# Kernel tuning notes

Hardware: AMD Instinct MI355X
Metric: run time of the kernel (lower is better)

Reference implementation:

```python
import jax, jax.numpy as jnp
import numpy as np

BETA = 0.25  # commitment loss weight (standard VQ-VAE)


def setup_inputs() -> dict:
    key = jax.random.key(0)
    ks = jax.random.split(key, 6)
    B, C, H, W = 8, 64, 64, 64
    K = 8192  # codebook size
    return {
        "z": jax.random.normal(ks[0], (B, C, H, W), dtype=jnp.float32),
        "pre_w": jax.random.normal(ks[1], (C, C), dtype=jnp.float32) * (1.0 / np.sqrt(C)),
        "pre_b": jax.random.normal(ks[2], (C,), dtype=jnp.float32) * 0.02,
        "emb": jax.random.normal(ks[3], (K, C), dtype=jnp.float32),
        "post_w": jax.random.normal(ks[4], (C, C), dtype=jnp.float32) * (1.0 / np.sqrt(C)),
        "post_b": jax.random.normal(ks[5], (C,), dtype=jnp.float32) * 0.02,
    }


def reference(z, pre_w, pre_b, emb, post_w, post_b):
    B, C, H, W = z.shape
    # pre_quant_conv: 1x1 conv == channel-mixing matmul
    ze = jnp.einsum("bchw,oc->bohw", z, pre_w) + pre_b[None, :, None, None]
    # flatten to tokens [N, C]
    zf = ze.transpose(0, 2, 3, 1).reshape(-1, C)
    # squared L2 distances to codebook: ||z||^2 - 2 z.e + ||e||^2
    d = (jnp.sum(zf * zf, axis=1, keepdims=True)
         - 2.0 * (zf @ emb.T)
         + jnp.sum(emb * emb, axis=1)[None, :])  # [N, K]
    idx = jnp.argmin(d, axis=1)  # [N]
    q = emb[idx].reshape(B, H, W, C).transpose(0, 3, 1, 2)  # [B,C,H,W]
    # VQ losses
    codebook_loss = jnp.mean((jax.lax.stop_gradient(ze) - q) ** 2)
    commit_loss = BETA * jnp.mean((ze - jax.lax.stop_gradient(q)) ** 2)
    loss = codebook_loss + commit_loss
    # straight-through estimator
    quant = ze + jax.lax.stop_gradient(q - ze)
    # post_quant_conv: 1x1 conv
    out = jnp.einsum("bchw,oc->bohw", quant, post_w) + post_b[None, :, None, None]
    return out, loss
```

## Files before the change

### kernel.cpp

```cpp
#include <hip/hip_runtime.h>
#include <stdint.h>

#define HW 4096
#define NTOK 32768
#define KCB 8192
#define YSPLIT 8
#define KCOV (KCB / YSPLIT)
#define NCHUNK (KCOV / 64)
#define MARGIN 0.01f

typedef __bf16 bf16x8 __attribute__((ext_vector_type(8)));
typedef float f32x16 __attribute__((ext_vector_type(16)));
typedef unsigned int uint;
typedef unsigned short u16;
typedef unsigned long long u64;

static __device__ inline u16 f2bf(float f) {
    uint u = __float_as_uint(f);
    return (u16)((u + 0x7FFFu + ((u >> 16) & 1u)) >> 16);
}
static __device__ inline float bf2f(u16 h) {
    return __uint_as_float(((uint)h) << 16);
}
static __device__ inline uint fsort(float f) {
    uint u = __float_as_uint(f);
    return u ^ ((uint)((int)u >> 31) | 0x80000000u);
}
static __device__ inline float funsort(uint s) {
    uint m = (s & 0x80000000u) ? 0x80000000u : 0xFFFFFFFFu;
    return __uint_as_float(s ^ m);
}

__global__ __launch_bounds__(256) void embprep_kernel(
    const float* __restrict__ emb, u16* __restrict__ embq,
    float* __restrict__ ee, int* __restrict__ flagcnt)
{
    const int t   = threadIdx.x;
    const int k   = blockIdx.x * 32 + (t >> 3);
    const int sub = t & 7;
    const float4* er = (const float4*)(emb + (size_t)k * 64 + sub * 8);
    float4 v0 = er[0], v1 = er[1];

    float s = v0.x*v0.x + v0.y*v0.y + v0.z*v0.z + v0.w*v0.w
            + v1.x*v1.x + v1.y*v1.y + v1.z*v1.z + v1.w*v1.w;
    s += __shfl_xor(s, 1, 64);
    s += __shfl_xor(s, 2, 64);
    s += __shfl_xor(s, 4, 64);
    if (sub == 0) ee[k] = s;

    float vals[8] = {-2.f*v0.x, -2.f*v0.y, -2.f*v0.z, -2.f*v0.w,
                     -2.f*v1.x, -2.f*v1.y, -2.f*v1.z, -2.f*v1.w};
    u16 hb[8], lb[8];
    #pragma unroll
    for (int c = 0; c < 8; ++c) {
        hb[c] = f2bf(vals[c]);
        lb[c] = f2bf(vals[c] - bf2f(hb[c]));
    }
    uint4 uh, ul;
    uh.x = (uint)hb[0] | ((uint)hb[1] << 16);
    uh.y = (uint)hb[2] | ((uint)hb[3] << 16);
    uh.z = (uint)hb[4] | ((uint)hb[5] << 16);
    uh.w = (uint)hb[6] | ((uint)hb[7] << 16);
    ul.x = (uint)lb[0] | ((uint)lb[1] << 16);
    ul.y = (uint)lb[2] | ((uint)lb[3] << 16);
    ul.z = (uint)lb[4] | ((uint)lb[5] << 16);
    ul.w = (uint)lb[6] | ((uint)lb[7] << 16);

    const int sw = k & 7;
    uint4* out = (uint4*)(embq + (size_t)k * 128);
    out[sub ^ sw]       = uh;
    out[(8 + sub) ^ sw] = ul;
    if (k == 0 && t == 0) *flagcnt = 0;
}

__global__ __launch_bounds__(256) void preconv_kernel(
    const float* __restrict__ z, const float* __restrict__ pre_w,
    const float* __restrict__ pre_b, u16* __restrict__ zq)
{
    __shared__ __attribute__((aligned(16))) float wt[64 * 64];
    __shared__ __attribute__((aligned(16))) float zt[64 * 64];
    __shared__ float bls[64];
    const int t = threadIdx.x;
    const int tok0 = blockIdx.x * 64;
    const int b    = tok0 >> 12;
    const int hw0  = tok0 & 4095;

    for (int i = t; i < 64 * 64; i += 256) {
        int o = i >> 6, c = i & 63;
        wt[c * 64 + o] = pre_w[i];
    }
    if (t < 64) bls[t] = pre_b[t];
    {
        const int tl = t & 63;
        #pragma unroll
        for (int rr = 0; rr < 16; ++rr) {
            const int c = (t >> 6) + rr * 4;
            zt[c * 64 + tl] = z[(size_t)b * (64 * HW) + (size_t)c * HW + hw0 + tl];
        }
    }
    __syncthreads();

    const int tok = t >> 2;
    const int og  = t & 3;
    const int n   = tok0 + tok;

    float acc[16];
    #pragma unroll
    for (int j = 0; j < 16; ++j) acc[j] = 0.f;

    for (int c = 0; c < 64; ++c) {
        const float zv = zt[c * 64 + tok];
        #pragma unroll
        for (int g = 0; g < 4; ++g) {
            float4 w4 = *(const float4*)(wt + c * 64 + og * 16 + g * 4);
            acc[g*4+0] = fmaf(zv, w4.x, acc[g*4+0]);
            acc[g*4+1] = fmaf(zv, w4.y, acc[g*4+1]);
            acc[g*4+2] = fmaf(zv, w4.z, acc[g*4+2]);
            acc[g*4+3] = fmaf(zv, w4.w, acc[g*4+3]);
        }
    }
    #pragma unroll
    for (int j = 0; j < 16; ++j) acc[j] += bls[og * 16 + j];

    uint uh[8], ul[8];
    #pragma unroll
    for (int j = 0; j < 8; ++j) {
        float v0 = acc[2*j], v1 = acc[2*j+1];
        u16 h0 = f2bf(v0), h1 = f2bf(v1);
        u16 l0 = f2bf(v0 - bf2f(h0)), l1 = f2bf(v1 - bf2f(h1));
        uh[j] = (uint)h0 | ((uint)h1 << 16);
        ul[j] = (uint)l0 | ((uint)l1 << 16);
    }
    uint4* zh = (uint4*)(zq + (size_t)n * 128 + og * 16);
    uint4* zl = (uint4*)(zq + (size_t)n * 128 + 64 + og * 16);
    zh[0] = *(uint4*)&uh[0]; zh[1] = *(uint4*)&uh[4];
    zl[0] = *(uint4*)&ul[0]; zl[1] = *(uint4*)&ul[4];
}

__global__ __launch_bounds__(256, 3) void dist_kernel(
    const u16* __restrict__ zq, const u16* __restrict__ embq,
    const float* __restrict__ ee, u64* __restrict__ halfkey,
    float* __restrict__ halfsec)
{
    __shared__ __attribute__((aligned(16))) char smem[32768];
    __shared__ u64 gbk[128];

    const int t    = threadIdx.x;
    const int w    = t >> 6;
    const int l    = t & 63;
    const int col  = l & 31;
    const int half = l >> 5;
    const int tok0 = blockIdx.x * 128;
    const int y    = blockIdx.y;
    const int kbase = y * KCOV;

    bf16x8 ah[4], al[4];
    {
        const u16* zrow = zq + (size_t)(tok0 + w * 32 + col) * 128;
        #pragma unroll
        for (int s = 0; s < 4; ++s) {
            ah[s] = *(const bf16x8*)(zrow + s*16 + half*8);
            al[s] = *(const bf16x8*)(zrow + 64 + s*16 + half*8);
        }
    }

    const int sw = col & 7;
    int boh[4][2], bol[4][2];
    #pragma unroll
    for (int s = 0; s < 4; ++s)
        #pragma unroll
        for (int ct = 0; ct < 2; ++ct) {
            const int nl = ct * 32 + col;
            boh[s][ct] = nl * 256 + (((s*2 + half) ^ sw) << 4);
            bol[s][ct] = nl * 256 + (((8 + s*2 + half) ^ sw) << 4);
        }

    float bb[16], ss[16]; uint ii[16];
    #pragma unroll
    for (int r = 0; r < 16; ++r) { bb[r] = 3.0e38f; ss[r] = 3.0e38f; ii[r] = 0; }

    float e0 = ee[kbase + col];
    float e1 = ee[kbase + 32 + col];
    uint cb0 = (uint)(kbase + col);
    uint cb1 = cb0 + 32;

    {
        const char* g = (const char*)embq + (size_t)kbase * 256;
        #pragma unroll
        for (int i = 0; i < 4; ++i) {
            int off = i * 4096 + t * 16;
            __builtin_amdgcn_global_load_lds(
                (const __attribute__((address_space(1))) void*)(g + off),
                (__attribute__((address_space(3))) void*)(smem + off), 16, 0, 0);
        }
    }

    for (int kt = 0; kt < NCHUNK; ++kt) {
        __syncthreads();
        if (kt + 1 < NCHUNK) {
            const char* g = (const char*)embq + (size_t)kbase * 256 + (size_t)(kt + 1) * 16384;
            char* ld = smem + ((kt + 1) & 1) * 16384;
            #pragma unroll
            for (int i = 0; i < 4; ++i) {
                int off = i * 4096 + t * 16;
                __builtin_amdgcn_global_load_lds(
                    (const __attribute__((address_space(1))) void*)(g + off),
                    (__attribute__((address_space(3))) void*)(ld + off), 16, 0, 0);
            }
        }
        const char* buf = smem + (kt & 1) * 16384;

        float e0n = 0.f, e1n = 0.f;
        if (kt + 1 < NCHUNK) {
            e0n = ee[kbase + (kt+1)*64 + col];
            e1n = ee[kbase + (kt+1)*64 + 32 + col];
        }

        f32x16 a0, a1;
        #pragma unroll
        for (int r = 0; r < 16; ++r) { a0[r] = e0; a1[r] = e1; }

        #pragma unroll
        for (int s = 0; s < 4; ++s) {
            bf16x8 bh0 = *(const bf16x8*)(buf + boh[s][0]);
            bf16x8 bh1 = *(const bf16x8*)(buf + boh[s][1]);
            bf16x8 bl0 = *(const bf16x8*)(buf + bol[s][0]);
            bf16x8 bl1 = *(const bf16x8*)(buf + bol[s][1]);
            a0 = __builtin_amdgcn_mfma_f32_32x32x16_bf16(ah[s], bh0, a0, 0, 0, 0);
            a1 = __builtin_amdgcn_mfma_f32_32x32x16_bf16(ah[s], bh1, a1, 0, 0, 0);
            a0 = __builtin_amdgcn_mfma_f32_32x32x16_bf16(ah[s], bl0, a0, 0, 0, 0);
            a1 = __builtin_amdgcn_mfma_f32_32x32x16_bf16(ah[s], bl1, a1, 0, 0, 0);
            a0 = __builtin_amdgcn_mfma_f32_32x32x16_bf16(al[s], bh0, a0, 0, 0, 0);
            a1 = __builtin_amdgcn_mfma_f32_32x32x16_bf16(al[s], bh1, a1, 0, 0, 0);
        }

        #pragma unroll
        for (int r = 0; r < 16; ++r) {
            float d0 = a0[r], d1 = a1[r];
            float lo = fminf(d0, d1);
            uint i01 = (d1 < d0) ? cb1 : cb0;
            ii[r] = (lo < bb[r]) ? i01 : ii[r];
            ss[r] = fminf(ss[r], __builtin_amdgcn_fmed3f(bb[r], d0, d1));
            bb[r] = fminf(bb[r], lo);
        }
        e0 = e0n; e1 = e1n;
        cb0 += 64; cb1 += 64;
    }

    __syncthreads();
    u64* keyt = (u64*)smem;
    #pragma unroll
    for (int r = 0; r < 16; ++r) {
        const int tw = (r & 3) + 8 * (r >> 2) + 4 * half;
        keyt[(w * 32 + tw) * 32 + col] = ((u64)fsort(bb[r]) << 32) | ii[r];
    }
    __syncthreads();
    if (t < 128) {
        u64 gb = keyt[t * 32 + (t & 31)];
        for (int j = 1; j < 32; ++j) {
            u64 v = keyt[t * 32 + ((j + t) & 31)];
            if (v < gb) gb = v;
        }
        gbk[t] = gb;
    }
    __syncthreads();
    float* svt = (float*)smem;
    #pragma unroll
    for (int r = 0; r < 16; ++r) {
        const int tw = (r & 3) + 8 * (r >> 2) + 4 * half;
        const int tl = w * 32 + tw;
        u64 mykey = ((u64)fsort(bb[r]) << 32) | ii[r];
        svt[tl * 32 + col] = (mykey == gbk[tl]) ? ss[r] : bb[r];
    }
    __syncthreads();
    if (t < 128) {
        float sv = 3.0e38f;
        for (int j = 0; j < 32; ++j)
            sv = fminf(sv, svt[t * 32 + ((j + t) & 31)]);
        halfkey[(size_t)y * NTOK + tok0 + t] = gbk[t];
        halfsec[(size_t)y * NTOK + tok0 + t] = sv;
    }
}

__global__ __launch_bounds__(256) void merge_kernel(
    const u64* __restrict__ halfkey, const float* __restrict__ halfsec,
    u64* __restrict__ bestkey, int* __restrict__ flagcnt,
    int* __restrict__ flaglist)
{
    const int n = blockIdx.x * 256 + threadIdx.x;
    u64 m1 = ~0ull, m2 = ~0ull;
    float smin = 3.0e38f;
    #pragma unroll
    for (int y = 0; y < YSPLIT; ++y) {
        u64 k = halfkey[(size_t)y * NTOK + n];
        u64 hi = (k > m1) ? k : m1;
        m1 = (k < m1) ? k : m1;
        m2 = (hi < m2) ? hi : m2;
        smin = fminf(smin, halfsec[(size_t)y * NTOK + n]);
    }
    const float bv = funsort((uint)(m1 >> 32));
    const float sv = fminf(smin, funsort((uint)(m2 >> 32)));
    const bool flag = (sv - bv < MARGIN);
    bestkey[n] = flag ? ~0ull : m1;
    if (flag) {
        int pos = atomicAdd(flagcnt, 1);
        flaglist[pos] = n;
    }
}

__global__ __launch_bounds__(256) void cleanup_kernel(
    const u16* __restrict__ zq, const float* __restrict__ emb,
    const float* __restrict__ ee, const int* __restrict__ flagcnt,
    const int* __restrict__ flaglist, u64* __restrict__ bestkey)
{
    __shared__ __attribute__((aligned(16))) float zf[64];
    __shared__ u64 smin;
    const int cnt = *flagcnt;
    const int t = threadIdx.x;

    for (int job = blockIdx.x; job < cnt * 32; job += 2048) {
        const int fi    = job >> 5;
        const int slice = job & 31;
        const int tok   = flaglist[fi];
        if (t == 0) smin = ~0ull;
        if (t < 64) {
            const u16* zr = zq + (size_t)tok * 128;
            zf[t] = bf2f(zr[t]) + bf2f(zr[64 + t]);
        }
        __syncthreads();

        const int k = slice * 256 + t;
        const float4* er = (const float4*)(emb + (size_t)k * 64);
        float d = 0.f;
        #pragma unroll
        for (int jj = 0; jj < 16; ++jj) {
            float4 e = er[jj];
            float4 zv = *(const float4*)&zf[4*jj];
            d = fmaf(e.x, zv.x, fmaf(e.y, zv.y, fmaf(e.z, zv.z, fmaf(e.w, zv.w, d))));
        }
        float dd = fmaf(-2.f, d, ee[k]);
        u64 key = ((u64)fsort(dd) << 32) | (uint)k;
        #pragma unroll
        for (int off = 32; off > 0; off >>= 1) {
            u64 o = __shfl_down(key, off, 64);
            key = (o < key) ? o : key;
        }
        if ((t & 63) == 0) atomicMin(&smin, key);
        __syncthreads();
        if (t == 0) atomicMin(&bestkey[tok], smin);
        __syncthreads();
    }
}

__global__ __launch_bounds__(256) void gather_kernel(
    const float* __restrict__ emb, const u64* __restrict__ bestkey,
    const u16* __restrict__ zq, const float* __restrict__ post_w,
    const float* __restrict__ post_b, float* __restrict__ out,
    float* __restrict__ lossp)
{
    __shared__ __attribute__((aligned(16))) float wt[64 * 64];
    __shared__ __attribute__((aligned(16))) float qt[64 * 64];
    __shared__ float bls[64];
    __shared__ int idxs[64];
    __shared__ float red[4];
    const int t = threadIdx.x;
    const int tok0 = blockIdx.x * 64;
    const int b    = tok0 >> 12;
    const int hw0  = tok0 & 4095;

    for (int i = t; i < 64 * 64; i += 256) {
        int o = i >> 6, c = i & 63;
        wt[c * 64 + o] = post_w[i];
    }
    if (t < 64) {
        bls[t] = post_b[t];
        idxs[t] = (int)(bestkey[tok0 + t] & 0xFFFFFFFFull);
    }
    __syncthreads();

    const int tok = t >> 2;
    const int og  = t & 3;
    const int n   = tok0 + tok;

    {
        const float4* qr = (const float4*)(emb + (size_t)idxs[tok] * 64);
        #pragma unroll
        for (int p = 0; p < 4; ++p) {
            const int c0 = og * 16 + p * 4;
            float4 v = qr[c0 >> 2];
            qt[(c0+0) * 64 + tok] = v.x;
            qt[(c0+1) * 64 + tok] = v.y;
            qt[(c0+2) * 64 + tok] = v.z;
            qt[(c0+3) * 64 + tok] = v.w;
        }
    }
    __syncthreads();

    float acc[16];
    #pragma unroll
    for (int j = 0; j < 16; ++j) acc[j] = 0.f;

    for (int c = 0; c < 64; ++c) {
        const float qv = qt[c * 64 + tok];
        #pragma unroll
        for (int g = 0; g < 4; ++g) {
            float4 w4 = *(const float4*)(wt + c * 64 + og * 16 + g * 4);
            acc[g*4+0] = fmaf(qv, w4.x, acc[g*4+0]);
            acc[g*4+1] = fmaf(qv, w4.y, acc[g*4+1]);
            acc[g*4+2] = fmaf(qv, w4.z, acc[g*4+2]);
            acc[g*4+3] = fmaf(qv, w4.w, acc[g*4+3]);
        }
    }

    float* op = out + (size_t)b * (64 * HW) + hw0 + tok;
    #pragma unroll
    for (int j = 0; j < 16; ++j)
        op[(size_t)(og * 16 + j) * HW] = acc[j] + bls[og * 16 + j];

    float lsum = 0.f;
    {
        const uint4* zh = (const uint4*)(zq + (size_t)n * 128 + og * 16);
        const uint4* zl = (const uint4*)(zq + (size_t)n * 128 + 64 + og * 16);
        #pragma unroll
        for (int h = 0; h < 2; ++h) {
            uint4 uh = zh[h], ul = zl[h];
            const uint uhv[4] = {uh.x, uh.y, uh.z, uh.w};
            const uint ulv[4] = {ul.x, ul.y, ul.z, ul.w};
            #pragma unroll
            for (int p = 0; p < 4; ++p) {
                const int c = og * 16 + h * 8 + p * 2;
                float z0 = bf2f((u16)(uhv[p] & 0xFFFF)) + bf2f((u16)(ulv[p] & 0xFFFF));
                float z1 = bf2f((u16)(uhv[p] >> 16))    + bf2f((u16)(ulv[p] >> 16));
                float d0 = z0 - qt[c * 64 + tok];
                float d1 = z1 - qt[(c + 1) * 64 + tok];
                lsum += d0 * d0 + d1 * d1;
            }
        }
    }
    #pragma unroll
    for (int off = 32; off > 0; off >>= 1) lsum += __shfl_down(lsum, off, 64);
    if ((t & 63) == 0) red[t >> 6] = lsum;
    __syncthreads();
    if (t == 0) lossp[blockIdx.x] = red[0] + red[1] + red[2] + red[3];
}

__global__ void lossred_kernel(const float* __restrict__ lossp, float* __restrict__ loss_out)
{
    __shared__ double sd[256];
    const int t = threadIdx.x;
    sd[t] = (double)lossp[t] + (double)lossp[t + 256];
    __syncthreads();
    for (int off = 128; off > 0; off >>= 1) {
        if (t < off) sd[t] += sd[t + off];
        __syncthreads();
    }
    if (t == 0)
        loss_out[0] = (float)(1.25 * sd[0] / (double)((size_t)NTOK * 64));
}

extern "C" void kernel_launch(void* const* d_in, const int* in_sizes, int n_in,
                              void* d_out, int out_size, void* d_ws, size_t ws_size,
                              hipStream_t stream)
{
    const float* z      = (const float*)d_in[0];
    const float* pre_w  = (const float*)d_in[1];
    const float* pre_b  = (const float*)d_in[2];
    const float* emb    = (const float*)d_in[3];
    const float* post_w = (const float*)d_in[4];
    const float* post_b = (const float*)d_in[5];
    float* outp = (float*)d_out;

    u16*   zq       = (u16*)d_ws;
    float* ee       = (float*)(zq + (size_t)NTOK * 128);
    u16*   embq     = (u16*)(ee + KCB);
    u64*   bestkey  = (u64*)(embq + (size_t)KCB * 128);
    int*   flagcnt  = (int*)(bestkey + NTOK);
    int*   flaglist = flagcnt + 1;
    float* lossp    = (float*)(flaglist + NTOK);
    u64*   halfkey  = (u64*)(lossp + 512);
    float* halfsec  = (float*)(halfkey + (size_t)YSPLIT * NTOK);

    embprep_kernel<<<KCB / 32, 256, 0, stream>>>(emb, embq, ee, flagcnt);
    preconv_kernel<<<NTOK / 64, 256, 0, stream>>>(z, pre_w, pre_b, zq);
    dist_kernel<<<dim3(NTOK / 128, YSPLIT), 256, 0, stream>>>(zq, embq, ee, halfkey, halfsec);
    merge_kernel<<<NTOK / 256, 256, 0, stream>>>(halfkey, halfsec, bestkey, flagcnt, flaglist);
    cleanup_kernel<<<2048, 256, 0, stream>>>(zq, emb, ee, flagcnt, flaglist, bestkey);
    gather_kernel<<<NTOK / 64, 256, 0, stream>>>(emb, bestkey, zq, post_w, post_b, outp, lossp);
    lossred_kernel<<<1, 256, 0, stream>>>(lossp, outp + (size_t)NTOK * 64);
}
```

Baseline: 237.4 us.

## Double token tile in dist kernel, pack index into distance bits, fuse loss reduction

Each dist block now handles 256 tokens with two 32-token groups per wave, so every codebook fragment read from LDS feeds twice as many MFMAs. Distances are offset by 256 so they stay positive, and the local code index is stored in the low 10 mantissa bits, which turns the argmin into plain unsigned min with half-width keys. The ambiguity margin is widened to scale with the exponent to cover the truncated bits. The final loss reduction kernel is replaced by float atomics into the output. The costs are higher register pressure (launch bounds drop to 2 blocks per SIMD), float atomics that make the loss sum order nondeterministic, and possibly more tokens sent to the exact cleanup pass.

```diff
diff --git a/kernel.cpp b/kernel.cpp
--- a/kernel.cpp
+++ b/kernel.cpp
@@ -7,7 +7,6 @@
 #define YSPLIT 8
 #define KCOV (KCB / YSPLIT)
 #define NCHUNK (KCOV / 64)
-#define MARGIN 0.01f
 
 typedef __bf16 bf16x8 __attribute__((ext_vector_type(8)));
 typedef float f32x16 __attribute__((ext_vector_type(16)));
@@ -26,14 +25,15 @@
     uint u = __float_as_uint(f);
     return u ^ ((uint)((int)u >> 31) | 0x80000000u);
 }
-static __device__ inline float funsort(uint s) {
-    uint m = (s & 0x80000000u) ? 0x80000000u : 0xFFFFFFFFu;
-    return __uint_as_float(s ^ m);
+static __device__ inline uint umin2(uint a, uint b) { return a < b ? a : b; }
+static __device__ inline uint umax2(uint a, uint b) { return a > b ? a : b; }
+static __device__ inline uint umed3(uint a, uint b, uint c) {
+    return umax2(umin2(a, b), umin2(umax2(a, b), c));
 }
 
 __global__ __launch_bounds__(256) void embprep_kernel(
     const float* __restrict__ emb, u16* __restrict__ embq,
-    float* __restrict__ ee, int* __restrict__ flagcnt)
+    float* __restrict__ ee, float* __restrict__ eeb, int* __restrict__ flagcnt)
 {
     const int t   = threadIdx.x;
     const int k   = blockIdx.x * 32 + (t >> 3);
@@ -46,7 +46,7 @@
     s += __shfl_xor(s, 1, 64);
     s += __shfl_xor(s, 2, 64);
     s += __shfl_xor(s, 4, 64);
-    if (sub == 0) ee[k] = s;
+    if (sub == 0) { ee[k] = s; eeb[k] = 256.f + s; }
 
     float vals[8] = {-2.f*v0.x, -2.f*v0.y, -2.f*v0.z, -2.f*v0.w,
                      -2.f*v1.x, -2.f*v1.y, -2.f*v1.z, -2.f*v1.w};
@@ -137,30 +137,31 @@
     zl[0] = *(uint4*)&ul[0]; zl[1] = *(uint4*)&ul[4];
 }
 
-__global__ __launch_bounds__(256, 3) void dist_kernel(
+__global__ __launch_bounds__(256, 2) void dist_kernel(
     const u16* __restrict__ zq, const u16* __restrict__ embq,
-    const float* __restrict__ ee, u64* __restrict__ halfkey,
-    float* __restrict__ halfsec)
+    const float* __restrict__ eeb, uint* __restrict__ halfbb,
+    uint* __restrict__ halfss)
 {
     __shared__ __attribute__((aligned(16))) char smem[32768];
-    __shared__ u64 gbk[128];
+    __shared__ uint gbk[256];
 
     const int t    = threadIdx.x;
     const int w    = t >> 6;
     const int l    = t & 63;
     const int col  = l & 31;
     const int half = l >> 5;
-    const int tok0 = blockIdx.x * 128;
+    const int tok0 = blockIdx.x * 256;
     const int y    = blockIdx.y;
     const int kbase = y * KCOV;
 
-    bf16x8 ah[4], al[4];
-    {
-        const u16* zrow = zq + (size_t)(tok0 + w * 32 + col) * 128;
+    bf16x8 ah[2][4], al[2][4];
+    #pragma unroll
+    for (int g = 0; g < 2; ++g) {
+        const u16* zrow = zq + (size_t)(tok0 + w * 64 + g * 32 + col) * 128;
         #pragma unroll
         for (int s = 0; s < 4; ++s) {
-            ah[s] = *(const bf16x8*)(zrow + s*16 + half*8);
-            al[s] = *(const bf16x8*)(zrow + 64 + s*16 + half*8);
+            ah[g][s] = *(const bf16x8*)(zrow + s*16 + half*8);
+            al[g][s] = *(const bf16x8*)(zrow + 64 + s*16 + half*8);
         }
     }
 
@@ -175,14 +176,12 @@
             bol[s][ct] = nl * 256 + (((8 + s*2 + half) ^ sw) << 4);
         }
 
-    float bb[16], ss[16]; uint ii[16];
-    #pragma unroll
-    for (int r = 0; r < 16; ++r) { bb[r] = 3.0e38f; ss[r] = 3.0e38f; ii[r] = 0; }
-
-    float e0 = ee[kbase + col];
-    float e1 = ee[kbase + 32 + col];
-    uint cb0 = (uint)(kbase + col);
-    uint cb1 = cb0 + 32;
+    uint bb[32], ss[32];
+    #pragma unroll
+    for (int q = 0; q < 32; ++q) { bb[q] = 0xFFFFFFFFu; ss[q] = 0xFFFFFFFFu; }
+
+    float e0 = eeb[kbase + col];
+    float e1 = eeb[kbase + 32 + col];
 
     {
         const char* g = (const char*)embq + (size_t)kbase * 256;
@@ -212,13 +211,13 @@
 
         float e0n = 0.f, e1n = 0.f;
         if (kt + 1 < NCHUNK) {
-            e0n = ee[kbase + (kt+1)*64 + col];
-            e1n = ee[kbase + (kt+1)*64 + 32 + col];
-        }
-
-        f32x16 a0, a1;
-        #pragma unroll
-        for (int r = 0; r < 16; ++r) { a0[r] = e0; a1[r] = e1; }
+            e0n = eeb[kbase + (kt+1)*64 + col];
+            e1n = eeb[kbase + (kt+1)*64 + 32 + col];
+        }
+
+        f32x16 a00, a01, a10, a11;
+        #pragma unroll
+        for (int r = 0; r < 16; ++r) { a00[r] = e0; a01[r] = e1; a10[r] = e0; a11[r] = e1; }
 
         #pragma unroll
         for (int s = 0; s < 4; ++s) {
@@ -226,92 +225,110 @@
             bf16x8 bh1 = *(const bf16x8*)(buf + boh[s][1]);
             bf16x8 bl0 = *(const bf16x8*)(buf + bol[s][0]);
             bf16x8 bl1 = *(const bf16x8*)(buf + bol[s][1]);
-            a0 = __builtin_amdgcn_mfma_f32_32x32x16_bf16(ah[s], bh0, a0, 0, 0, 0);
-            a1 = __builtin_amdgcn_mfma_f32_32x32x16_bf16(ah[s], bh1, a1, 0, 0, 0);
-            a0 = __builtin_amdgcn_mfma_f32_32x32x16_bf16(ah[s], bl0, a0, 0, 0, 0);
-            a1 = __builtin_amdgcn_mfma_f32_32x32x16_bf16(ah[s], bl1, a1, 0, 0, 0);
-            a0 = __builtin_amdgcn_mfma_f32_32x32x16_bf16(al[s], bh0, a0, 0, 0, 0);
-            a1 = __builtin_amdgcn_mfma_f32_32x32x16_bf16(al[s], bh1, a1, 0, 0, 0);
-        }
-
+            a00 = __builtin_amdgcn_mfma_f32_32x32x16_bf16(ah[0][s], bh0, a00, 0, 0, 0);
+            a01 = __builtin_amdgcn_mfma_f32_32x32x16_bf16(ah[0][s], bh1, a01, 0, 0, 0);
+            a10 = __builtin_amdgcn_mfma_f32_32x32x16_bf16(ah[1][s], bh0, a10, 0, 0, 0);
+            a11 = __builtin_amdgcn_mfma_f32_32x32x16_bf16(ah[1][s], bh1, a11, 0, 0, 0);
+            a00 = __builtin_amdgcn_mfma_f32_32x32x16_bf16(ah[0][s], bl0, a00, 0, 0, 0);
+            a01 = __builtin_amdgcn_mfma_f32_32x32x16_bf16(ah[0][s], bl1, a01, 0, 0, 0);
+            a10 = __builtin_amdgcn_mfma_f32_32x32x16_bf16(ah[1][s], bl0, a10, 0, 0, 0);
+            a11 = __builtin_amdgcn_mfma_f32_32x32x16_bf16(ah[1][s], bl1, a11, 0, 0, 0);
+            a00 = __builtin_amdgcn_mfma_f32_32x32x16_bf16(al[0][s], bh0, a00, 0, 0, 0);
+            a01 = __builtin_amdgcn_mfma_f32_32x32x16_bf16(al[0][s], bh1, a01, 0, 0, 0);
+            a10 = __builtin_amdgcn_mfma_f32_32x32x16_bf16(al[1][s], bh0, a10, 0, 0, 0);
+            a11 = __builtin_amdgcn_mfma_f32_32x32x16_bf16(al[1][s], bh1, a11, 0, 0, 0);
+        }
+
+        const uint i0 = (uint)(kt * 64 + col);
+        const uint i1 = i0 + 32;
+        #pragma unroll
+        for (int g = 0; g < 2; ++g) {
+            #pragma unroll
+            for (int r = 0; r < 16; ++r) {
+                const float d0 = g ? a10[r] : a00[r];
+                const float d1 = g ? a11[r] : a01[r];
+                const uint p0 = (__float_as_uint(d0) & 0xFFFFFC00u) | i0;
+                const uint p1 = (__float_as_uint(d1) & 0xFFFFFC00u) | i1;
+                const int q = g * 16 + r;
+                ss[q] = umin2(ss[q], umed3(bb[q], p0, p1));
+                bb[q] = umin2(umin2(bb[q], p0), p1);
+            }
+        }
+        e0 = e0n; e1 = e1n;
+    }
+
+    __syncthreads();
+    uint* keyt = (uint*)smem;
+    #pragma unroll
+    for (int g = 0; g < 2; ++g)
         #pragma unroll
         for (int r = 0; r < 16; ++r) {
-            float d0 = a0[r], d1 = a1[r];
-            float lo = fminf(d0, d1);
-            uint i01 = (d1 < d0) ? cb1 : cb0;
-            ii[r] = (lo < bb[r]) ? i01 : ii[r];
-            ss[r] = fminf(ss[r], __builtin_amdgcn_fmed3f(bb[r], d0, d1));
-            bb[r] = fminf(bb[r], lo);
-        }
-        e0 = e0n; e1 = e1n;
-        cb0 += 64; cb1 += 64;
-    }
-
-    __syncthreads();
-    u64* keyt = (u64*)smem;
-    #pragma unroll
-    for (int r = 0; r < 16; ++r) {
-        const int tw = (r & 3) + 8 * (r >> 2) + 4 * half;
-        keyt[(w * 32 + tw) * 32 + col] = ((u64)fsort(bb[r]) << 32) | ii[r];
-    }
-    __syncthreads();
-    if (t < 128) {
-        u64 gb = keyt[t * 32 + (t & 31)];
-        for (int j = 1; j < 32; ++j) {
-            u64 v = keyt[t * 32 + ((j + t) & 31)];
-            if (v < gb) gb = v;
-        }
+            const int tl = w*64 + g*32 + (r & 3) + 8*(r >> 2) + 4*half;
+            keyt[tl * 32 + col] = bb[g*16 + r];
+        }
+    __syncthreads();
+    {
+        uint gb = keyt[t * 32 + (t & 31)];
+        #pragma unroll 4
+        for (int j = 1; j < 32; ++j)
+            gb = umin2(gb, keyt[t * 32 + ((j + t) & 31)]);
         gbk[t] = gb;
     }
     __syncthreads();
-    float* svt = (float*)smem;
-    #pragma unroll
-    for (int r = 0; r < 16; ++r) {
-        const int tw = (r & 3) + 8 * (r >> 2) + 4 * half;
-        const int tl = w * 32 + tw;
-        u64 mykey = ((u64)fsort(bb[r]) << 32) | ii[r];
-        svt[tl * 32 + col] = (mykey == gbk[tl]) ? ss[r] : bb[r];
-    }
-    __syncthreads();
-    if (t < 128) {
-        float sv = 3.0e38f;
-        for (int j = 0; j < 32; ++j)
-            sv = fminf(sv, svt[t * 32 + ((j + t) & 31)]);
-        halfkey[(size_t)y * NTOK + tok0 + t] = gbk[t];
-        halfsec[(size_t)y * NTOK + tok0 + t] = sv;
+    #pragma unroll
+    for (int g = 0; g < 2; ++g)
+        #pragma unroll
+        for (int r = 0; r < 16; ++r) {
+            const int tl = w*64 + g*32 + (r & 3) + 8*(r >> 2) + 4*half;
+            const uint mykey = bb[g*16 + r];
+            keyt[tl * 32 + col] = (mykey == gbk[tl]) ? ss[g*16 + r] : mykey;
+        }
+    __syncthreads();
+    {
+        uint sv = keyt[t * 32 + (t & 31)];
+        #pragma unroll 4
+        for (int j = 1; j < 32; ++j)
+            sv = umin2(sv, keyt[t * 32 + ((j + t) & 31)]);
+        halfbb[(size_t)y * NTOK + tok0 + t] = gbk[t];
+        halfss[(size_t)y * NTOK + tok0 + t] = sv;
     }
 }
 
 __global__ __launch_bounds__(256) void merge_kernel(
-    const u64* __restrict__ halfkey, const float* __restrict__ halfsec,
-    u64* __restrict__ bestkey, int* __restrict__ flagcnt,
-    int* __restrict__ flaglist)
+    const uint* __restrict__ halfbb, const uint* __restrict__ halfss,
+    uint* __restrict__ bestidx, u64* __restrict__ bestkeyB,
+    int* __restrict__ flagcnt, int* __restrict__ flaglist,
+    float* __restrict__ loss_out)
 {
     const int n = blockIdx.x * 256 + threadIdx.x;
-    u64 m1 = ~0ull, m2 = ~0ull;
-    float smin = 3.0e38f;
+    uint m1 = 0xFFFFFFFFu, m2 = 0xFFFFFFFFu, smin = 0xFFFFFFFFu;
+    int ywin = 0;
     #pragma unroll
     for (int y = 0; y < YSPLIT; ++y) {
-        u64 k = halfkey[(size_t)y * NTOK + n];
-        u64 hi = (k > m1) ? k : m1;
-        m1 = (k < m1) ? k : m1;
-        m2 = (hi < m2) ? hi : m2;
-        smin = fminf(smin, halfsec[(size_t)y * NTOK + n]);
-    }
-    const float bv = funsort((uint)(m1 >> 32));
-    const float sv = fminf(smin, funsort((uint)(m2 >> 32)));
-    const bool flag = (sv - bv < MARGIN);
-    bestkey[n] = flag ? ~0ull : m1;
+        const uint kb = halfbb[(size_t)y * NTOK + n];
+        if (kb < m1) { m2 = m1; m1 = kb; ywin = y; }
+        else if (kb < m2) m2 = kb;
+        smin = umin2(smin, halfss[(size_t)y * NTOK + n]);
+    }
+    const uint secb = umin2(m2, smin) & 0xFFFFFC00u;
+    const float bv = __uint_as_float(m1 & 0xFFFFFC00u);
+    const float sv = __uint_as_float(secb);
+    const float p2 = __uint_as_float(__float_as_uint(sv) & 0x7F800000u);
+    const float margin = 0.002f + p2 * 4.8828125e-4f;
+    const bool flag = (sv - bv) < margin;
+    bestidx[n]  = flag ? 0xFFFFFFFFu : (uint)(ywin * 1024) + (m1 & 1023u);
+    bestkeyB[n] = ~0ull;
     if (flag) {
         int pos = atomicAdd(flagcnt, 1);
         flaglist[pos] = n;
     }
+    if (n == 0) loss_out[0] = 0.f;
 }
 
 __global__ __launch_bounds__(256) void cleanup_kernel(
     const u16* __restrict__ zq, const float* __restrict__ emb,
     const float* __restrict__ ee, const int* __restrict__ flagcnt,
-    const int* __restrict__ flaglist, u64* __restrict__ bestkey)
+    const int* __restrict__ flaglist, u64* __restrict__ bestkeyB)
 {
     __shared__ __attribute__((aligned(16))) float zf[64];
     __shared__ u64 smin;
@@ -347,16 +364,16 @@
         }
         if ((t & 63) == 0) atomicMin(&smin, key);
         __syncthreads();
-        if (t == 0) atomicMin(&bestkey[tok], smin);
+        if (t == 0) atomicMin(&bestkeyB[tok], smin);
         __syncthreads();
     }
 }
 
 __global__ __launch_bounds__(256) void gather_kernel(
-    const float* __restrict__ emb, const u64* __restrict__ bestkey,
-    const u16* __restrict__ zq, const float* __restrict__ post_w,
-    const float* __restrict__ post_b, float* __restrict__ out,
-    float* __restrict__ lossp)
+    const float* __restrict__ emb, const uint* __restrict__ bestidx,
+    const u64* __restrict__ bestkeyB, const u16* __restrict__ zq,
+    const float* __restrict__ post_w, const float* __restrict__ post_b,
+    float* __restrict__ out, float* __restrict__ loss_out)
 {
     __shared__ __attribute__((aligned(16))) float wt[64 * 64];
     __shared__ __attribute__((aligned(16))) float qt[64 * 64];
@@ -374,7 +391,9 @@
     }
     if (t < 64) {
         bls[t] = post_b[t];
-        idxs[t] = (int)(bestkey[tok0 + t] & 0xFFFFFFFFull);
+        const uint raw = bestidx[tok0 + t];
+        idxs[t] = (raw == 0xFFFFFFFFu) ? (int)(bestkeyB[tok0 + t] & 0xFFFFFFFFull)
+                                       : (int)raw;
     }
     __syncthreads();
 
@@ -441,21 +460,10 @@
     for (int off = 32; off > 0; off >>= 1) lsum += __shfl_down(lsum, off, 64);
     if ((t & 63) == 0) red[t >> 6] = lsum;
     __syncthreads();
-    if (t == 0) lossp[blockIdx.x] = red[0] + red[1] + red[2] + red[3];
-}
-
-__global__ void lossred_kernel(const float* __restrict__ lossp, float* __restrict__ loss_out)
-{
-    __shared__ double sd[256];
-    const int t = threadIdx.x;
-    sd[t] = (double)lossp[t] + (double)lossp[t + 256];
-    __syncthreads();
-    for (int off = 128; off > 0; off >>= 1) {
-        if (t < off) sd[t] += sd[t + off];
-        __syncthreads();
-    }
-    if (t == 0)
-        loss_out[0] = (float)(1.25 * sd[0] / (double)((size_t)NTOK * 64));
+    if (t == 0) {
+        const float tot = red[0] + red[1] + red[2] + red[3];
+        atomicAdd(loss_out, tot * (1.25f / 2097152.f));
+    }
 }
 
 extern "C" void kernel_launch(void* const* d_in, const int* in_sizes, int n_in,
@@ -469,22 +477,25 @@
     const float* post_w = (const float*)d_in[4];
     const float* post_b = (const float*)d_in[5];
     float* outp = (float*)d_out;
+    float* loss_out = outp + (size_t)NTOK * 64;
 
     u16*   zq       = (u16*)d_ws;
     float* ee       = (float*)(zq + (size_t)NTOK * 128);
-    u16*   embq     = (u16*)(ee + KCB);
-    u64*   bestkey  = (u64*)(embq + (size_t)KCB * 128);
-    int*   flagcnt  = (int*)(bestkey + NTOK);
+    float* eeb      = ee + KCB;
+    u16*   embq     = (u16*)(eeb + KCB);
+    u64*   bestkeyB = (u64*)(embq + (size_t)KCB * 128);
+    uint*  bestidx  = (uint*)(bestkeyB + NTOK);
+    int*   flagcnt  = (int*)(bestidx + NTOK);
     int*   flaglist = flagcnt + 1;
-    float* lossp    = (float*)(flaglist + NTOK);
-    u64*   halfkey  = (u64*)(lossp + 512);
-    float* halfsec  = (float*)(halfkey + (size_t)YSPLIT * NTOK);
-
-    embprep_kernel<<<KCB / 32, 256, 0, stream>>>(emb, embq, ee, flagcnt);
+    uint*  halfbb   = (uint*)(flaglist + NTOK);
+    uint*  halfss   = halfbb + (size_t)YSPLIT * NTOK;
+
+    embprep_kernel<<<KCB / 32, 256, 0, stream>>>(emb, embq, ee, eeb, flagcnt);
     preconv_kernel<<<NTOK / 64, 256, 0, stream>>>(z, pre_w, pre_b, zq);
-    dist_kernel<<<dim3(NTOK / 128, YSPLIT), 256, 0, stream>>>(zq, embq, ee, halfkey, halfsec);
-    merge_kernel<<<NTOK / 256, 256, 0, stream>>>(halfkey, halfsec, bestkey, flagcnt, flaglist);
-    cleanup_kernel<<<2048, 256, 0, stream>>>(zq, emb, ee, flagcnt, flaglist, bestkey);
-    gather_kernel<<<NTOK / 64, 256, 0, stream>>>(emb, bestkey, zq, post_w, post_b, outp, lossp);
-    lossred_kernel<<<1, 256, 0, stream>>>(lossp, outp + (size_t)NTOK * 64);
-}
+    dist_kernel<<<dim3(NTOK / 256, YSPLIT), 256, 0, stream>>>(zq, embq, eeb, halfbb, halfss);
+    merge_kernel<<<NTOK / 256, 256, 0, stream>>>(halfbb, halfss, bestidx, bestkeyB,
+                                                 flagcnt, flaglist, loss_out);
+    cleanup_kernel<<<2048, 256, 0, stream>>>(zq, emb, ee, flagcnt, flaglist, bestkeyB);
+    gather_kernel<<<NTOK / 64, 256, 0, stream>>>(emb, bestidx, bestkeyB, zq,
+                                                 post_w, post_b, outp, loss_out);
+}
```

Result: slower. 459.8 us (+93.7%).
